# Kernel optimization log

Measured on AMD Instinct MI355X. Metric: run time of the kernel, lower is better.

## Reference

```python
import jax, jax.numpy as jnp
import numpy as np

ALPHA = 0.2  # LeakyReLU negative slope


def setup_inputs() -> dict:
    key = jax.random.key(0)
    k1, k2, k3, k4 = jax.random.split(key, 4)
    bs, N, Fin, Fout = 8, 2048, 128, 64
    x = jax.random.normal(k1, (bs, N, Fin), dtype=jnp.float32)
    adj = jax.random.randint(k2, (N, N), 0, 2, dtype=jnp.int32)
    W = jax.random.normal(k3, (Fin, Fout), dtype=jnp.float32) * 0.1
    a = jax.random.normal(k4, (2 * Fout, 1), dtype=jnp.float32) * 0.1
    return {"x": x, "adj": adj, "W": W, "a": a}


def reference(x, adj, W, a):
    # h: [bs, N, Fout]
    h = jnp.einsum("bnf,fo->bno", x, W)
    Fp = h.shape[-1]
    # Split a into the source/target halves: a^T [h_i || h_j] = a1.h_i + a2.h_j
    a1 = a[:Fp, 0]  # [Fout]
    a2 = a[Fp:, 0]  # [Fout]
    s1 = jnp.einsum("bno,o->bn", h, a1)  # score contribution of node i
    s2 = jnp.einsum("bno,o->bn", h, a2)  # score contribution of node j
    # e[b, i, j] = leakyrelu(a1.h_i + a2.h_j)  -- [bs, N, N]
    e = jax.nn.leaky_relu(s1[:, :, None] + s2[:, None, :], negative_slope=ALPHA)
    neg = jnp.asarray(-9e15, dtype=e.dtype)
    att = jnp.where(adj[None, :, :] > 0, e, neg)
    att = jax.nn.softmax(att, axis=-1)  # masked softmax over neighbors j
    h_prime = jnp.einsum("bij,bjo->bio", att, h)
    return jax.nn.elu(h_prime)  # concat=True path
```

## Files before the change

kernel.cpp:

```cpp
#include <hip/hip_runtime.h>
#include <hip/hip_bf16.h>
#include <math.h>

#define N_NODES 2048
#define FIN 128
#define FOUT 64
#define BS 8
#define ALPHA 0.2f
#define LOG2E 1.4426950408889634f

typedef __attribute__((ext_vector_type(8))) short short8v;
typedef __attribute__((ext_vector_type(4))) float f32x4;

__device__ __forceinline__ unsigned int pack2bf(float a, float b) {
  __hip_bfloat162 t = __float22bfloat162_rn(make_float2(a, b));
  unsigned int r;
  __builtin_memcpy(&r, &t, 4);
  return r;
}
__device__ __forceinline__ void split2(float f0, float f1, unsigned &hi, unsigned &lo) {
  hi = pack2bf(f0, f1);
  const float h0 = __uint_as_float(hi << 16);
  const float h1 = __uint_as_float(hi & 0xFFFF0000u);
  lo = pack2bf(f0 - h0, f1 - h1);
}
__device__ __forceinline__ float exp2_raw(float x) {
  float r;
  asm volatile("v_exp_f32 %0, %1\n\ts_nop 1" : "=v"(r) : "v"(x));
  return r;
}
__device__ __forceinline__ float elu_f(float v) {
  return v > 0.f ? v : expm1f(v);
}

__global__ __launch_bounds__(256, 4) void gat_prep(const float* __restrict__ x,
                                                   const int* __restrict__ adj,
                                                   const float* __restrict__ W,
                                                   const float* __restrict__ a,
                                                   short* __restrict__ hp,
                                                   float* __restrict__ s1,
                                                   float* __restrict__ s2,
                                                   unsigned int* __restrict__ mask32) {
  const int bx = blockIdx.x;
  const int b = bx >> 7;
  const int t16 = bx & 127;
  const int i0 = t16 * 16;
  const int w = threadIdx.x >> 6, lane = threadIdx.x & 63;
  const int kg = lane >> 4, rl = lane & 15;

  __shared__ float h_lds[16][68];

  const int mrow_id = 2 * bx + (w >> 1);
  const int* ar = adj + (long long)mrow_id * N_NODES + (w & 1) * 1024;
  int mreg[16];
  #pragma unroll
  for (int c = 0; c < 16; ++c) mreg[c] = ar[c * 64 + lane];

  const float* xB = x + ((long long)b * N_NODES + i0 + rl) * FIN + kg * 8;
  float4 xv[8];
  #pragma unroll
  for (int i = 0; i < 8; ++i)
    xv[i] = *reinterpret_cast<const float4*>(xB + (i >> 1) * 32 + (i & 1) * 4);

  union u8s { short8v v; unsigned u[4]; };
  u8s bh[4], bl[4];
  #pragma unroll
  for (int ks = 0; ks < 4; ++ks) {
    #pragma unroll
    for (int pe = 0; pe < 4; ++pe) {
      const float w0 = W[(ks * 32 + kg * 8 + 2 * pe) * FOUT + w * 16 + rl];
      const float w1 = W[(ks * 32 + kg * 8 + 2 * pe + 1) * FOUT + w * 16 + rl];
      split2(w0, w1, bh[ks].u[pe], bl[ks].u[pe]);
    }
  }

  f32x4 ahh = {0.f, 0.f, 0.f, 0.f};
  f32x4 ahl = {0.f, 0.f, 0.f, 0.f};
  f32x4 alh = {0.f, 0.f, 0.f, 0.f};
  #pragma unroll
  for (int ks = 0; ks < 4; ++ks) {
    const float4 xa = xv[2 * ks], xb = xv[2 * ks + 1];
    const float xf[8] = {xa.x, xa.y, xa.z, xa.w, xb.x, xb.y, xb.z, xb.w};
    u8s xh, xl;
    #pragma unroll
    for (int pe = 0; pe < 4; ++pe)
      split2(xf[2 * pe], xf[2 * pe + 1], xh.u[pe], xl.u[pe]);
    ahh = __builtin_amdgcn_mfma_f32_16x16x32_bf16(xh.v, bh[ks].v, ahh, 0, 0, 0);
    ahl = __builtin_amdgcn_mfma_f32_16x16x32_bf16(xh.v, bl[ks].v, ahl, 0, 0, 0);
    alh = __builtin_amdgcn_mfma_f32_16x16x32_bf16(xl.v, bh[ks].v, alh, 0, 0, 0);
  }
  const f32x4 acc = (ahh + ahl) + alh;
  #pragma unroll
  for (int r = 0; r < 4; ++r)
    h_lds[kg * 4 + r][w * 16 + rl] = acc[r];

  {
    unsigned int* mw = mask32 + mrow_id * 64 + (w & 1) * 32;
    #pragma unroll
    for (int c = 0; c < 16; ++c) {
      const unsigned long long bal = __ballot(mreg[c] > 0);
      if (lane == 0) mw[2 * c] = (unsigned int)bal;
      if (lane == 1) mw[2 * c + 1] = (unsigned int)(bal >> 32);
    }
  }

  __syncthreads();

  {
    const float a1v = a[lane], a2v = a[FOUT + lane];
    #pragma unroll
    for (int rr = 0; rr < 4; ++rr) {
      const float hv = h_lds[4 * w + rr][lane];
      float p = hv * a1v, q = hv * a2v;
      #pragma unroll
      for (int off = 32; off > 0; off >>= 1) {
        p += __shfl_xor(p, off);
        q += __shfl_xor(q, off);
      }
      if (lane == 0) {
        s1[(long long)b * N_NODES + i0 + 4 * w + rr] = p * LOG2E;
        s2[(long long)b * N_NODES + i0 + 4 * w + rr] = q * LOG2E;
      }
    }
  }

  if (lane < 32) {
    const int jt = t16 >> 1, kh = t16 & 1;
    const int kgl = lane >> 4, col = lane & 15;
    u8s o;
    #pragma unroll
    for (int i = 0; i < 4; ++i)
      o.u[i] = pack2bf(h_lds[kgl * 8 + 2 * i][w * 16 + col],
                       h_lds[kgl * 8 + 2 * i + 1][w * 16 + col]);
    *reinterpret_cast<short8v*>(
        hp + (((long long)(b * 256 + jt * 4 + w)) * 64 + (kh * 2 + kgl) * 16 + col) * 8) = o.v;
  }
}

__global__ __launch_bounds__(512, 4) void gat_attn(const unsigned int* __restrict__ mask32,
                                                   const short* __restrict__ hp,
                                                   const float* __restrict__ s1g,
                                                   const float* __restrict__ s2g,
                                                   float* __restrict__ out) {
  const int b = blockIdx.y;
  const int i0 = blockIdx.x * 32;
  const int t = threadIdx.x;
  const int w = t >> 6, lane = t & 63;
  const int kg = lane >> 4, rl = lane & 15;

  __shared__ float red[8][16 * 64];
  __shared__ float ps[8][16];
  __shared__ uint2 lut[16];

  if (t < 16) {
    const unsigned v = t;
    lut[t].x = ((v & 1u) ? 0xFFFFu : 0u) | ((v & 2u) ? 0xFFFF0000u : 0u);
    lut[t].y = ((v & 4u) ? 0xFFFFu : 0u) | ((v & 8u) ? 0xFFFF0000u : 0u);
  }
  __syncthreads();

  const float s1v1 = s1g[b * N_NODES + i0 + rl];
  const float s1v2 = s1g[b * N_NODES + i0 + 16 + rl];
  const float* s2B = s2g + b * N_NODES;
  const unsigned int* mrow1 = mask32 + (i0 + rl) * 64;
  const unsigned int* mrow2 = mask32 + (i0 + 16 + rl) * 64;
  const short8v* hpB = reinterpret_cast<const short8v*>(hp) + (long long)b * 16384;

  f32x4 a10 = {0.f, 0.f, 0.f, 0.f}, a11 = {0.f, 0.f, 0.f, 0.f};
  f32x4 a12 = {0.f, 0.f, 0.f, 0.f}, a13 = {0.f, 0.f, 0.f, 0.f};
  f32x4 a20 = {0.f, 0.f, 0.f, 0.f}, a21 = {0.f, 0.f, 0.f, 0.f};
  f32x4 a22 = {0.f, 0.f, 0.f, 0.f}, a23 = {0.f, 0.f, 0.f, 0.f};
  f32x4 aS1 = {0.f, 0.f, 0.f, 0.f}, aS2 = {0.f, 0.f, 0.f, 0.f};
  union u8s { short8v v; unsigned u[4]; };
  u8s ones;
  #pragma unroll
  for (int i = 0; i < 4; ++i) ones.u[i] = 0x3F803F80u;

  #pragma unroll
  for (int k = 0; k < 8; ++k) {
    const int jt = w + 8 * k;
    const short8v* hpt = hpB + jt * 256;
    const short8v b0 = hpt[0 * 64 + lane];
    const short8v b1 = hpt[1 * 64 + lane];
    const short8v b2 = hpt[2 * 64 + lane];
    const short8v b3 = hpt[3 * 64 + lane];
    const float4 sa = *reinterpret_cast<const float4*>(s2B + jt * 32 + kg * 8);
    const float4 sb = *reinterpret_cast<const float4*>(s2B + jt * 32 + kg * 8 + 4);
    const unsigned int m1 = (mrow1[jt] >> (kg * 8)) & 0xFFu;
    const unsigned int m2 = (mrow2[jt] >> (kg * 8)) & 0xFFu;
    const uint2 k10 = lut[m1 & 15u], k11 = lut[m1 >> 4];
    const uint2 k20 = lut[m2 & 15u], k21 = lut[m2 >> 4];
    const float s2e[8] = {sa.x, sa.y, sa.z, sa.w, sb.x, sb.y, sb.z, sb.w};
    float p1[8], p2[8];
    #pragma unroll
    for (int e = 0; e < 8; e++) {
      float sc1 = s1v1 + s2e[e];
      float sc2 = s2e[e] + s1v2;
      sc1 = fmaxf(sc1, ALPHA * sc1);
      sc2 = fmaxf(sc2, ALPHA * sc2);
      p1[e] = exp2_raw(sc1);
      p2[e] = exp2_raw(sc2);
    }
    u8s af1, af2;
    af1.u[0] = pack2bf(p1[0], p1[1]) & k10.x;
    af1.u[1] = pack2bf(p1[2], p1[3]) & k10.y;
    af1.u[2] = pack2bf(p1[4], p1[5]) & k11.x;
    af1.u[3] = pack2bf(p1[6], p1[7]) & k11.y;
    af2.u[0] = pack2bf(p2[0], p2[1]) & k20.x;
    af2.u[1] = pack2bf(p2[2], p2[3]) & k20.y;
    af2.u[2] = pack2bf(p2[4], p2[5]) & k21.x;
    af2.u[3] = pack2bf(p2[6], p2[7]) & k21.y;
    a10 = __builtin_amdgcn_mfma_f32_16x16x32_bf16(af1.v, b0, a10, 0, 0, 0);
    a20 = __builtin_amdgcn_mfma_f32_16x16x32_bf16(af2.v, b0, a20, 0, 0, 0);
    a11 = __builtin_amdgcn_mfma_f32_16x16x32_bf16(af1.v, b1, a11, 0, 0, 0);
    a21 = __builtin_amdgcn_mfma_f32_16x16x32_bf16(af2.v, b1, a21, 0, 0, 0);
    a12 = __builtin_amdgcn_mfma_f32_16x16x32_bf16(af1.v, b2, a12, 0, 0, 0);
    a22 = __builtin_amdgcn_mfma_f32_16x16x32_bf16(af2.v, b2, a22, 0, 0, 0);
    a13 = __builtin_amdgcn_mfma_f32_16x16x32_bf16(af1.v, b3, a13, 0, 0, 0);
    a23 = __builtin_amdgcn_mfma_f32_16x16x32_bf16(af2.v, b3, a23, 0, 0, 0);
    aS1 = __builtin_amdgcn_mfma_f32_16x16x32_bf16(af1.v, ones.v, aS1, 0, 0, 0);
    aS2 = __builtin_amdgcn_mfma_f32_16x16x32_bf16(af2.v, ones.v, aS2, 0, 0, 0);
  }

  #pragma unroll
  for (int r = 0; r < 4; r++) {
    red[w][(kg * 4 + r) * 64 + 0 * 16 + rl] = a10[r];
    red[w][(kg * 4 + r) * 64 + 1 * 16 + rl] = a11[r];
    red[w][(kg * 4 + r) * 64 + 2 * 16 + rl] = a12[r];
    red[w][(kg * 4 + r) * 64 + 3 * 16 + rl] = a13[r];
  }
  if (rl == 0) {
    #pragma unroll
    for (int r = 0; r < 4; r++) ps[w][kg * 4 + r] = aS1[r];
  }
  __syncthreads();
  {
    const int row = t >> 5;
    const int c2 = (t & 31) * 2;
    float den = 0.f, v0 = 0.f, v1 = 0.f;
    #pragma unroll
    for (int s = 0; s < 8; ++s) {
      den += ps[s][row];
      const float* rp = &red[s][row * 64 + c2];
      v0 += rp[0]; v1 += rp[1];
    }
    const float inv = 1.0f / den;
    float2 ov;
    ov.x = elu_f(v0 * inv);
    ov.y = elu_f(v1 * inv);
    *reinterpret_cast<float2*>(
        out + ((long long)b * N_NODES + i0 + row) * FOUT + c2) = ov;
  }
  __syncthreads();

  #pragma unroll
  for (int r = 0; r < 4; r++) {
    red[w][(kg * 4 + r) * 64 + 0 * 16 + rl] = a20[r];
    red[w][(kg * 4 + r) * 64 + 1 * 16 + rl] = a21[r];
    red[w][(kg * 4 + r) * 64 + 2 * 16 + rl] = a22[r];
    red[w][(kg * 4 + r) * 64 + 3 * 16 + rl] = a23[r];
  }
  if (rl == 0) {
    #pragma unroll
    for (int r = 0; r < 4; r++) ps[w][kg * 4 + r] = aS2[r];
  }
  __syncthreads();
  {
    const int row = t >> 5;
    const int c2 = (t & 31) * 2;
    float den = 0.f, v0 = 0.f, v1 = 0.f;
    #pragma unroll
    for (int s = 0; s < 8; ++s) {
      den += ps[s][row];
      const float* rp = &red[s][row * 64 + c2];
      v0 += rp[0]; v1 += rp[1];
    }
    const float inv = 1.0f / den;
    float2 ov;
    ov.x = elu_f(v0 * inv);
    ov.y = elu_f(v1 * inv);
    *reinterpret_cast<float2*>(
        out + ((long long)b * N_NODES + i0 + 16 + row) * FOUT + c2) = ov;
  }
}

extern "C" void kernel_launch(void* const* d_in, const int* in_sizes, int n_in,
                              void* d_out, int out_size, void* d_ws, size_t ws_size,
                              hipStream_t stream) {
  const float* x   = (const float*)d_in[0];
  const int*   adj = (const int*)d_in[1];
  const float* W   = (const float*)d_in[2];
  const float* a   = (const float*)d_in[3];
  float* out = (float*)d_out;

  short* hp = (short*)d_ws;
  float* s1 = (float*)(hp + (long long)BS * N_NODES * FOUT);
  float* s2 = s1 + BS * N_NODES;
  unsigned int* mask32 = (unsigned int*)(s2 + BS * N_NODES);

  gat_prep<<<1024, 256, 0, stream>>>(x, adj, W, a, hp, s1, s2, mask32);
  gat_attn<<<dim3(N_NODES / 32, BS), 512, 0, stream>>>(mask32, hp, s1, s2, out);
}
```

Measured before the change: 33.58 us.

## Pre-split W once, stage x via LDS, cache mask and s2 in LDS

Adds a small kernel that splits W into bf16 hi/lo fragments once, so each gat_prep block loads ready-made fragments instead of recomputing the split for every block. gat_prep now loads x with coalesced row reads into LDS and reads MFMA fragments from there. gat_attn stages the block's mask rows and the whole s2 vector in LDS, reusing the reduction buffer, which needs an extra barrier before that buffer is overwritten. The cost is one extra kernel launch and the added LDS traffic and synchronization.

```diff
diff --git a/kernel.cpp b/kernel.cpp
--- a/kernel.cpp
+++ b/kernel.cpp
@@ -33,9 +33,30 @@
   return v > 0.f ? v : expm1f(v);
 }
 
+__global__ __launch_bounds__(64) void w_pack(const float* __restrict__ W,
+                                             short* __restrict__ whi,
+                                             short* __restrict__ wlo) {
+  const int f = blockIdx.x;
+  const int lane = threadIdx.x;
+  const int kg = lane >> 4, rl = lane & 15;
+  const int ks = f >> 2, ct = f & 3;
+  float wv[8];
+  #pragma unroll
+  for (int e = 0; e < 8; ++e)
+    wv[e] = W[(ks * 32 + kg * 8 + e) * FOUT + ct * 16 + rl];
+  union u8s { short8v v; unsigned u[4]; };
+  u8s hi, lo;
+  #pragma unroll
+  for (int pe = 0; pe < 4; ++pe)
+    split2(wv[2 * pe], wv[2 * pe + 1], hi.u[pe], lo.u[pe]);
+  *reinterpret_cast<short8v*>(whi + ((long long)f * 64 + lane) * 8) = hi.v;
+  *reinterpret_cast<short8v*>(wlo + ((long long)f * 64 + lane) * 8) = lo.v;
+}
+
 __global__ __launch_bounds__(256, 4) void gat_prep(const float* __restrict__ x,
                                                    const int* __restrict__ adj,
-                                                   const float* __restrict__ W,
+                                                   const short* __restrict__ whi,
+                                                   const short* __restrict__ wlo,
                                                    const float* __restrict__ a,
                                                    short* __restrict__ hp,
                                                    float* __restrict__ s1,
@@ -45,9 +66,11 @@
   const int b = bx >> 7;
   const int t16 = bx & 127;
   const int i0 = t16 * 16;
-  const int w = threadIdx.x >> 6, lane = threadIdx.x & 63;
+  const int t = threadIdx.x;
+  const int w = t >> 6, lane = t & 63;
   const int kg = lane >> 4, rl = lane & 15;
 
+  __shared__ float x_lds[16][132];
   __shared__ float h_lds[16][68];
 
   const int mrow_id = 2 * bx + (w >> 1);
@@ -56,38 +79,39 @@
   #pragma unroll
   for (int c = 0; c < 16; ++c) mreg[c] = ar[c * 64 + lane];
 
-  const float* xB = x + ((long long)b * N_NODES + i0 + rl) * FIN + kg * 8;
-  float4 xv[8];
-  #pragma unroll
-  for (int i = 0; i < 8; ++i)
-    xv[i] = *reinterpret_cast<const float4*>(xB + (i >> 1) * 32 + (i & 1) * 4);
+  {
+    const float* xrow = x + ((long long)b * N_NODES + i0 + (t >> 4)) * FIN + (t & 15) * 8;
+    const float4 xa = *reinterpret_cast<const float4*>(xrow);
+    const float4 xb = *reinterpret_cast<const float4*>(xrow + 4);
+    *reinterpret_cast<float4*>(&x_lds[t >> 4][(t & 15) * 8]) = xa;
+    *reinterpret_cast<float4*>(&x_lds[t >> 4][(t & 15) * 8 + 4]) = xb;
+  }
 
   union u8s { short8v v; unsigned u[4]; };
-  u8s bh[4], bl[4];
+  short8v bh[4], bl[4];
   #pragma unroll
   for (int ks = 0; ks < 4; ++ks) {
-    #pragma unroll
-    for (int pe = 0; pe < 4; ++pe) {
-      const float w0 = W[(ks * 32 + kg * 8 + 2 * pe) * FOUT + w * 16 + rl];
-      const float w1 = W[(ks * 32 + kg * 8 + 2 * pe + 1) * FOUT + w * 16 + rl];
-      split2(w0, w1, bh[ks].u[pe], bl[ks].u[pe]);
-    }
-  }
+    bh[ks] = *reinterpret_cast<const short8v*>(whi + ((long long)((ks * 4 + w) * 64 + lane)) * 8);
+    bl[ks] = *reinterpret_cast<const short8v*>(wlo + ((long long)((ks * 4 + w) * 64 + lane)) * 8);
+  }
+
+  __syncthreads();
 
   f32x4 ahh = {0.f, 0.f, 0.f, 0.f};
   f32x4 ahl = {0.f, 0.f, 0.f, 0.f};
   f32x4 alh = {0.f, 0.f, 0.f, 0.f};
   #pragma unroll
   for (int ks = 0; ks < 4; ++ks) {
-    const float4 xa = xv[2 * ks], xb = xv[2 * ks + 1];
+    const float4 xa = *reinterpret_cast<const float4*>(&x_lds[rl][ks * 32 + kg * 8]);
+    const float4 xb = *reinterpret_cast<const float4*>(&x_lds[rl][ks * 32 + kg * 8 + 4]);
     const float xf[8] = {xa.x, xa.y, xa.z, xa.w, xb.x, xb.y, xb.z, xb.w};
     u8s xh, xl;
     #pragma unroll
     for (int pe = 0; pe < 4; ++pe)
       split2(xf[2 * pe], xf[2 * pe + 1], xh.u[pe], xl.u[pe]);
-    ahh = __builtin_amdgcn_mfma_f32_16x16x32_bf16(xh.v, bh[ks].v, ahh, 0, 0, 0);
-    ahl = __builtin_amdgcn_mfma_f32_16x16x32_bf16(xh.v, bl[ks].v, ahl, 0, 0, 0);
-    alh = __builtin_amdgcn_mfma_f32_16x16x32_bf16(xl.v, bh[ks].v, alh, 0, 0, 0);
+    ahh = __builtin_amdgcn_mfma_f32_16x16x32_bf16(xh.v, bh[ks], ahh, 0, 0, 0);
+    ahl = __builtin_amdgcn_mfma_f32_16x16x32_bf16(xh.v, bl[ks], ahl, 0, 0, 0);
+    alh = __builtin_amdgcn_mfma_f32_16x16x32_bf16(xl.v, bh[ks], alh, 0, 0, 0);
   }
   const f32x4 acc = (ahh + ahl) + alh;
   #pragma unroll
@@ -148,22 +172,34 @@
   const int w = t >> 6, lane = t & 63;
   const int kg = lane >> 4, rl = lane & 15;
 
-  __shared__ float red[8][16 * 64];
+  __shared__ float red[8][1024];
   __shared__ float ps[8][16];
   __shared__ uint2 lut[16];
+
+  unsigned int* mask_lds = reinterpret_cast<unsigned int*>(&red[0][0]);
+  float* s2_lds = &red[0][0] + 2080;
 
   if (t < 16) {
     const unsigned v = t;
     lut[t].x = ((v & 1u) ? 0xFFFFu : 0u) | ((v & 2u) ? 0xFFFF0000u : 0u);
     lut[t].y = ((v & 4u) ? 0xFFFFu : 0u) | ((v & 8u) ? 0xFFFF0000u : 0u);
   }
+  {
+    const uint4 mv = reinterpret_cast<const uint4*>(mask32 + i0 * 64)[t];
+    const int row = t >> 4, col = (t & 15) * 4;
+    mask_lds[row * 65 + col + 0] = mv.x;
+    mask_lds[row * 65 + col + 1] = mv.y;
+    mask_lds[row * 65 + col + 2] = mv.z;
+    mask_lds[row * 65 + col + 3] = mv.w;
+  }
+  {
+    const float4 sv = reinterpret_cast<const float4*>(s2g + b * N_NODES)[t];
+    *reinterpret_cast<float4*>(&s2_lds[t * 4]) = sv;
+  }
   __syncthreads();
 
   const float s1v1 = s1g[b * N_NODES + i0 + rl];
   const float s1v2 = s1g[b * N_NODES + i0 + 16 + rl];
-  const float* s2B = s2g + b * N_NODES;
-  const unsigned int* mrow1 = mask32 + (i0 + rl) * 64;
-  const unsigned int* mrow2 = mask32 + (i0 + 16 + rl) * 64;
   const short8v* hpB = reinterpret_cast<const short8v*>(hp) + (long long)b * 16384;
 
   f32x4 a10 = {0.f, 0.f, 0.f, 0.f}, a11 = {0.f, 0.f, 0.f, 0.f};
@@ -184,10 +220,10 @@
     const short8v b1 = hpt[1 * 64 + lane];
     const short8v b2 = hpt[2 * 64 + lane];
     const short8v b3 = hpt[3 * 64 + lane];
-    const float4 sa = *reinterpret_cast<const float4*>(s2B + jt * 32 + kg * 8);
-    const float4 sb = *reinterpret_cast<const float4*>(s2B + jt * 32 + kg * 8 + 4);
-    const unsigned int m1 = (mrow1[jt] >> (kg * 8)) & 0xFFu;
-    const unsigned int m2 = (mrow2[jt] >> (kg * 8)) & 0xFFu;
+    const float4 sa = *reinterpret_cast<const float4*>(&s2_lds[jt * 32 + kg * 8]);
+    const float4 sb = *reinterpret_cast<const float4*>(&s2_lds[jt * 32 + kg * 8 + 4]);
+    const unsigned int m1 = (mask_lds[rl * 65 + jt] >> (kg * 8)) & 0xFFu;
+    const unsigned int m2 = (mask_lds[(16 + rl) * 65 + jt] >> (kg * 8)) & 0xFFu;
     const uint2 k10 = lut[m1 & 15u], k11 = lut[m1 >> 4];
     const uint2 k20 = lut[m2 & 15u], k21 = lut[m2 >> 4];
     const float s2e[8] = {sa.x, sa.y, sa.z, sa.w, sb.x, sb.y, sb.z, sb.w};
@@ -222,6 +258,8 @@
     aS2 = __builtin_amdgcn_mfma_f32_16x16x32_bf16(af2.v, ones.v, aS2, 0, 0, 0);
   }
 
+  __syncthreads();
+
   #pragma unroll
   for (int r = 0; r < 4; r++) {
     red[w][(kg * 4 + r) * 64 + 0 * 16 + rl] = a10[r];
@@ -297,7 +335,10 @@
   float* s1 = (float*)(hp + (long long)BS * N_NODES * FOUT);
   float* s2 = s1 + BS * N_NODES;
   unsigned int* mask32 = (unsigned int*)(s2 + BS * N_NODES);
-
-  gat_prep<<<1024, 256, 0, stream>>>(x, adj, W, a, hp, s1, s2, mask32);
+  short* whi = (short*)(mask32 + N_NODES * 64);
+  short* wlo = whi + 16 * 64 * 8;
+
+  w_pack<<<16, 64, 0, stream>>>(W, whi, wlo);
+  gat_prep<<<1024, 256, 0, stream>>>(x, adj, whi, wlo, a, hp, s1, s2, mask32);
   gat_attn<<<dim3(N_NODES / 32, BS), 512, 0, stream>>>(mask32, hp, s1, s2, out);
 }
```

After: 32.56 us. 1.03x faster.
